# Performance work log

Measured on AMD Instinct MI355X. Metric: run time of the kernel, lower is better.

Reference implementation:

```python
import jax, jax.numpy as jnp
import numpy as np

TEMPERATURE = 1.0
N_ITER = 3
B, N_PATTERNS, N_NEURONS = 4096, 8192, 1024


def setup_inputs() -> dict:
    key = jax.random.key(0)
    kx, kp = jax.random.split(key)
    x = jax.random.normal(kx, (B, N_NEURONS), dtype=jnp.float32)
    # patterns initialized as tanh(randn * initial_variance) in the original module
    patterns = jnp.tanh(jax.random.normal(kp, (N_PATTERNS, N_NEURONS), dtype=jnp.float32) * 0.1)
    return {"x": x, "patterns": patterns}


def reference(x, patterns):
    # Iterative Hopfield update: x <- softmax(T * x @ P^T) @ P, repeated N_ITER times.
    def body(carry, _):
        scores = TEMPERATURE * jnp.einsum('bn,pn->bp', carry, patterns)  # [B, P]
        new_x = jnp.einsum('bp,pn->bn', jax.nn.softmax(scores, axis=1), patterns)  # [B, N]
        return new_x, None
    x, _ = jax.lax.scan(body, x, None, length=N_ITER)
    return x
```

## Files before the change

### kernel.cpp

```cpp
#include <hip/hip_runtime.h>
#include <hip/hip_fp16.h>
#include <stdint.h>

#define B_ROWS 4096
#define N_PAT  8192
#define N_NEU  1024

typedef _Float16 f16x8 __attribute__((ext_vector_type(8)));
typedef _Float16 f16x4 __attribute__((ext_vector_type(4)));
typedef float    f32x4 __attribute__((ext_vector_type(4)));

__device__ __forceinline__ f32x4 mfma16(f16x8 a, f16x8 b, f32x4 c) {
  return __builtin_amdgcn_mfma_f32_16x16x32_f16(a, b, c, 0, 0, 0);
}

__global__ __launch_bounds__(256) void convert_f32_f16(
    const float* __restrict__ in, _Float16* __restrict__ out, int n4) {
  int idx    = blockIdx.x * 256 + threadIdx.x;
  int stride = gridDim.x * 256;
  for (int i = idx; i < n4; i += stride) {
    float4 v = reinterpret_cast<const float4*>(in)[i];
    f16x4 h  = { (_Float16)v.x, (_Float16)v.y, (_Float16)v.z, (_Float16)v.w };
    reinterpret_cast<f16x4*>(out)[i] = h;
  }
}

__global__ __launch_bounds__(256) void transpose_f32_f16(
    const float* __restrict__ in, _Float16* __restrict__ out, int rows, int cols) {
  __shared__ float tile[32][33];
  int c0 = blockIdx.x * 32, r0 = blockIdx.y * 32;
  int tx = threadIdx.x, ty = threadIdx.y;
  #pragma unroll
  for (int i = 0; i < 32; i += 8)
    tile[ty + i][tx] = in[(size_t)(r0 + ty + i) * cols + c0 + tx];
  __syncthreads();
  #pragma unroll
  for (int i = 0; i < 32; i += 8)
    out[(size_t)(c0 + ty + i) * rows + r0 + tx] = (_Float16)tile[tx][ty + i];
}

__device__ __forceinline__ void gload_lds16(const _Float16* g, _Float16* l) {
  __builtin_amdgcn_global_load_lds(
      (const __attribute__((address_space(1))) uint32_t*)g,
      (__attribute__((address_space(3))) uint32_t*)l, 16, 0, 0);
}

template <typename OUT_T>
__global__ __launch_bounds__(512, 2) void gemm_x(
    const _Float16* __restrict__ A, const _Float16* __restrict__ Bt,
    OUT_T* __restrict__ C, int M, int N, int K, int KS) {
  __shared__ _Float16 lds[2][2][256 * 64];
  const int t    = threadIdx.x;
  const int lane = t & 63;
  const int w    = t >> 6;
  const int wr   = w >> 2;
  const int wc   = w & 3;
  const int m0   = blockIdx.x * 256;
  const int n0   = blockIdx.y * 256;
  const int k0   = blockIdx.z * KS;

  const int srow  = w * 8 + (lane >> 3);
  const int sgran = ((lane & 7) ^ ((lane >> 3) & 7)) * 8;
  const _Float16* sA = A  + (size_t)(m0 + srow) * K + sgran + k0;
  const _Float16* sB = Bt + (size_t)(n0 + srow) * K + sgran + k0;
  const size_t rj = (size_t)64 * K;
  const int ldst  = w * 512;

  const int lrow = lane & 15;
  const int kg   = lane >> 4;
  const int NT   = KS >> 6;

  f32x4 acc[8][4] = {};

  auto stage = [&](int slot, int kt) {
    #pragma unroll
    for (int j = 0; j < 4; ++j) {
      gload_lds16(sA + j * rj + kt, &lds[slot][0][j * 4096 + ldst]);
      gload_lds16(sB + j * rj + kt, &lds[slot][1][j * 4096 + ldst]);
    }
  };

  stage(0, 0);
  stage(1, 64);
  asm volatile("s_waitcnt vmcnt(8)" ::: "memory");
  __builtin_amdgcn_s_barrier();
  __builtin_amdgcn_sched_barrier(0);

  for (int tt = 0; tt < NT; ++tt) {
    const int s = tt & 1;
    const _Float16* As = lds[s][0];
    const _Float16* Bs = lds[s][1];

    f16x8 bf[4][2];
    #pragma unroll
    for (int ni = 0; ni < 4; ++ni) {
      const int br = wc * 64 + ni * 16 + lrow;
      #pragma unroll
      for (int ks = 0; ks < 2; ++ks)
        bf[ni][ks] = *reinterpret_cast<const f16x8*>(
            &Bs[br * 64 + (((ks * 4 + kg) ^ (br & 7)) * 8)]);
    }

    #pragma unroll
    for (int p = 0; p < 4; ++p) {
      f16x8 af[2][2];
      #pragma unroll
      for (int j = 0; j < 2; ++j) {
        const int ar = wr * 128 + (p * 2 + j) * 16 + lrow;
        #pragma unroll
        for (int ks = 0; ks < 2; ++ks)
          af[j][ks] = *reinterpret_cast<const f16x8*>(
              &As[ar * 64 + (((ks * 4 + kg) ^ (ar & 7)) * 8)]);
      }
      __builtin_amdgcn_s_setprio(1);
      #pragma unroll
      for (int j = 0; j < 2; ++j) {
        #pragma unroll
        for (int ni = 0; ni < 4; ++ni) {
          acc[p * 2 + j][ni] = mfma16(af[j][0], bf[ni][0], acc[p * 2 + j][ni]);
          acc[p * 2 + j][ni] = mfma16(af[j][1], bf[ni][1], acc[p * 2 + j][ni]);
        }
      }
      __builtin_amdgcn_s_setprio(0);
    }

    __builtin_amdgcn_s_barrier();
    __builtin_amdgcn_sched_barrier(0);
    if (tt + 2 < NT) {
      stage(s, (tt + 2) << 6);
      asm volatile("s_waitcnt vmcnt(8)" ::: "memory");
    } else {
      asm volatile("s_waitcnt vmcnt(0)" ::: "memory");
    }
    __builtin_amdgcn_s_barrier();
    __builtin_amdgcn_sched_barrier(0);
  }

  OUT_T* Cz = C + (size_t)blockIdx.z * M * N;
  const int crow = (lane >> 4) * 4;
  const int ccol = lane & 15;
  #pragma unroll
  for (int mi = 0; mi < 8; ++mi) {
    #pragma unroll
    for (int ni = 0; ni < 4; ++ni) {
      #pragma unroll
      for (int r = 0; r < 4; ++r) {
        int row = m0 + wr * 128 + mi * 16 + crow + r;
        int col = n0 + wc * 64 + ni * 16 + ccol;
        Cz[(size_t)row * N + col] = (OUT_T)acc[mi][ni][r];
      }
    }
  }
}

template <typename OUT_T, int SPLIT>
__global__ __launch_bounds__(256) void reduce_partials(
    const float* __restrict__ Cp, OUT_T* __restrict__ out, int n4, int stride4) {
  int idx    = blockIdx.x * 256 + threadIdx.x;
  int stride = gridDim.x * 256;
  for (int i = idx; i < n4; i += stride) {
    float4 a = reinterpret_cast<const float4*>(Cp)[i];
    #pragma unroll
    for (int s = 1; s < SPLIT; ++s) {
      float4 b = reinterpret_cast<const float4*>(Cp)[(size_t)s * stride4 + i];
      a.x += b.x; a.y += b.y; a.z += b.z; a.w += b.w;
    }
    if constexpr (sizeof(OUT_T) == 2) {
      f16x4 h = { (_Float16)a.x, (_Float16)a.y, (_Float16)a.z, (_Float16)a.w };
      reinterpret_cast<f16x4*>(out)[i] = h;
    } else {
      reinterpret_cast<float4*>(out)[i] = a;
    }
  }
}

__global__ __launch_bounds__(256) void softmax_rows(_Float16* __restrict__ S, int N) {
  const int t = threadIdx.x;
  f16x8* pv = reinterpret_cast<f16x8*>(S + (size_t)blockIdx.x * N);
  float v[32];
  float m = -3.0e38f;
  #pragma unroll
  for (int i = 0; i < 4; ++i) {
    f16x8 h = pv[i * 256 + t];
    #pragma unroll
    for (int e = 0; e < 8; ++e) {
      float f = (float)h[e];
      v[i * 8 + e] = f;
      m = fmaxf(m, f);
    }
  }
  #pragma unroll
  for (int o = 32; o; o >>= 1) m = fmaxf(m, __shfl_xor(m, o));
  __shared__ float redm[4];
  if ((t & 63) == 0) redm[t >> 6] = m;
  __syncthreads();
  m = fmaxf(fmaxf(redm[0], redm[1]), fmaxf(redm[2], redm[3]));

  float s = 0.f;
  #pragma unroll
  for (int i = 0; i < 32; ++i) { v[i] = __expf(v[i] - m); s += v[i]; }
  #pragma unroll
  for (int o = 32; o; o >>= 1) s += __shfl_xor(s, o);
  __shared__ float reds[4];
  if ((t & 63) == 0) reds[t >> 6] = s;
  __syncthreads();
  s = reds[0] + reds[1] + reds[2] + reds[3];
  const float inv = 1.0f / s;

  #pragma unroll
  for (int i = 0; i < 4; ++i) {
    f16x8 h;
    #pragma unroll
    for (int e = 0; e < 8; ++e) h[e] = (_Float16)(v[i * 8 + e] * inv);
    pv[i * 256 + t] = h;
  }
}

extern "C" void kernel_launch(void* const* d_in, const int* in_sizes, int n_in,
                              void* d_out, int out_size, void* d_ws, size_t ws_size,
                              hipStream_t stream) {
  const float* x        = (const float*)d_in[0];
  const float* patterns = (const float*)d_in[1];
  float* out            = (float*)d_out;
  char* ws = (char*)d_ws;

  _Float16* Xb   = (_Float16*)(ws);
  _Float16* Pb   = (_Float16*)(ws + ((size_t)8  << 20));
  _Float16* PbT  = (_Float16*)(ws + ((size_t)24 << 20));
  _Float16* S    = (_Float16*)(ws + ((size_t)40 << 20));
  float*    part = (float*)   (ws + ((size_t)104 << 20));

  const size_t base = (size_t)104 << 20;
  const int split = (ws_size >= base + ((size_t)64 << 20)) ? 4
                  : (ws_size >= base + ((size_t)32 << 20)) ? 2 : 1;

  convert_f32_f16<<<dim3(1024), dim3(256), 0, stream>>>(x, Xb, (B_ROWS * N_NEU) / 4);
  convert_f32_f16<<<dim3(2048), dim3(256), 0, stream>>>(patterns, Pb, (N_PAT * N_NEU) / 4);
  transpose_f32_f16<<<dim3(N_NEU / 32, N_PAT / 32), dim3(32, 8), 0, stream>>>(patterns, PbT, N_PAT, N_NEU);

  const int n4 = (B_ROWS * N_NEU) / 4;
  const int stride4 = n4;

  for (int it = 0; it < 3; ++it) {
    gemm_x<_Float16><<<dim3(B_ROWS / 256, N_PAT / 256, 1), dim3(512), 0, stream>>>(
        Xb, Pb, S, B_ROWS, N_PAT, N_NEU, N_NEU);
    softmax_rows<<<dim3(B_ROWS), dim3(256), 0, stream>>>(S, N_PAT);

    if (split > 1) {
      gemm_x<float><<<dim3(B_ROWS / 256, N_NEU / 256, split), dim3(512), 0, stream>>>(
          S, PbT, part, B_ROWS, N_NEU, N_PAT, N_PAT / split);
      if (it < 2) {
        if (split == 4)
          reduce_partials<_Float16, 4><<<dim3(2048), dim3(256), 0, stream>>>(part, Xb, n4, stride4);
        else
          reduce_partials<_Float16, 2><<<dim3(2048), dim3(256), 0, stream>>>(part, Xb, n4, stride4);
      } else {
        if (split == 4)
          reduce_partials<float, 4><<<dim3(2048), dim3(256), 0, stream>>>(part, out, n4, stride4);
        else
          reduce_partials<float, 2><<<dim3(2048), dim3(256), 0, stream>>>(part, out, n4, stride4);
      }
    } else {
      gemm_x<float><<<dim3(B_ROWS / 256, N_NEU / 256, 1), dim3(512), 0, stream>>>(
          S, PbT, part, B_ROWS, N_NEU, N_PAT, N_PAT);
      if (it < 2)
        reduce_partials<_Float16, 1><<<dim3(2048), dim3(256), 0, stream>>>(part, Xb, n4, stride4);
      else
        reduce_partials<float, 1><<<dim3(2048), dim3(256), 0, stream>>>(part, out, n4, stride4);
    }
  }
}
```

Measured before the change: 535.1 us.

## Interleave A/B tile prefetches across MFMA phases with per-phase barriers

Restructures the GEMM main loop so global-to-LDS loads for the next A tile and the tile after next for B are issued in halves between the four MFMA phases, instead of in one bulk stage after all compute. Each phase loads its A fragments, syncs with a barrier and lgkmcnt wait, then runs the MFMAs. The goal is to spread memory traffic across the compute and cut the idle time at iteration boundaries. It adds four extra barriers per K-step, and the split A/B buffering scheme overwrites buffers while other waves may still read them, which relies on the barrier placement being correct.

New measurement: 520.0 us. 2.8% less time.

```diff
diff --git a/kernel.cpp b/kernel.cpp
--- a/kernel.cpp
+++ b/kernel.cpp
@@ -72,68 +72,73 @@
 
   f32x4 acc[8][4] = {};
 
-  auto stage = [&](int slot, int kt) {
-    #pragma unroll
-    for (int j = 0; j < 4; ++j) {
-      gload_lds16(sA + j * rj + kt, &lds[slot][0][j * 4096 + ldst]);
-      gload_lds16(sB + j * rj + kt, &lds[slot][1][j * 4096 + ldst]);
-    }
+  auto stageAh = [&](int slot, int kt, int h) {
+    gload_lds16(sA + (size_t)(2 * h)     * rj + kt, &lds[slot][0][(2 * h)     * 4096 + ldst]);
+    gload_lds16(sA + (size_t)(2 * h + 1) * rj + kt, &lds[slot][0][(2 * h + 1) * 4096 + ldst]);
   };
-
-  stage(0, 0);
-  stage(1, 64);
-  asm volatile("s_waitcnt vmcnt(8)" ::: "memory");
-  __builtin_amdgcn_s_barrier();
-  __builtin_amdgcn_sched_barrier(0);
+  auto stageBh = [&](int slot, int kt, int h) {
+    gload_lds16(sB + (size_t)(2 * h)     * rj + kt, &lds[slot][1][(2 * h)     * 4096 + ldst]);
+    gload_lds16(sB + (size_t)(2 * h + 1) * rj + kt, &lds[slot][1][(2 * h + 1) * 4096 + ldst]);
+  };
+
+  stageBh(0, 0, 0);  stageBh(0, 0, 1);
+  stageAh(0, 0, 0);  stageAh(0, 0, 1);
+  stageBh(1, 64, 0); stageBh(1, 64, 1);
 
   for (int tt = 0; tt < NT; ++tt) {
     const int s = tt & 1;
+    if (tt + 1 < NT) asm volatile("s_waitcnt vmcnt(4)" ::: "memory");
+    else             asm volatile("s_waitcnt vmcnt(0)" ::: "memory");
+    __builtin_amdgcn_s_barrier();
+    __builtin_amdgcn_sched_barrier(0);
+
     const _Float16* As = lds[s][0];
     const _Float16* Bs = lds[s][1];
+    const int ktA  = (tt + 1) << 6;
+    const int ktB  = (tt + 2) << 6;
+    const bool pA  = (tt + 1 < NT);
+    const bool pB  = (tt + 2 < NT);
 
     f16x8 bf[4][2];
+
+#define PHASE_BODY(MI0)                                                              \
+    {                                                                                \
+      f16x8 a0, a1, a2, a3;                                                          \
+      { const int ar = wr * 128 + (MI0) * 16 + lrow;                                 \
+        a0 = *reinterpret_cast<const f16x8*>(&As[ar * 64 + (((kg) ^ (ar & 7)) * 8)]);      \
+        a1 = *reinterpret_cast<const f16x8*>(&As[ar * 64 + (((4 + kg) ^ (ar & 7)) * 8)]); }\
+      { const int ar = wr * 128 + ((MI0) + 1) * 16 + lrow;                           \
+        a2 = *reinterpret_cast<const f16x8*>(&As[ar * 64 + (((kg) ^ (ar & 7)) * 8)]);      \
+        a3 = *reinterpret_cast<const f16x8*>(&As[ar * 64 + (((4 + kg) ^ (ar & 7)) * 8)]); }\
+      __builtin_amdgcn_s_barrier();                                                  \
+      asm volatile("s_waitcnt lgkmcnt(0)" ::: "memory");                             \
+      __builtin_amdgcn_sched_barrier(0);                                             \
+      __builtin_amdgcn_s_setprio(1);                                                 \
+      _Pragma("unroll")                                                              \
+      for (int ni = 0; ni < 4; ++ni) {                                               \
+        acc[MI0][ni]       = mfma16(a0, bf[ni][0], acc[MI0][ni]);                    \
+        acc[MI0][ni]       = mfma16(a1, bf[ni][1], acc[MI0][ni]);                    \
+        acc[(MI0) + 1][ni] = mfma16(a2, bf[ni][0], acc[(MI0) + 1][ni]);              \
+        acc[(MI0) + 1][ni] = mfma16(a3, bf[ni][1], acc[(MI0) + 1][ni]);              \
+      }                                                                              \
+      __builtin_amdgcn_s_setprio(0);                                                 \
+    }
+
+    if (pA) stageAh(s ^ 1, ktA, 0);
     #pragma unroll
     for (int ni = 0; ni < 4; ++ni) {
       const int br = wc * 64 + ni * 16 + lrow;
-      #pragma unroll
-      for (int ks = 0; ks < 2; ++ks)
-        bf[ni][ks] = *reinterpret_cast<const f16x8*>(
-            &Bs[br * 64 + (((ks * 4 + kg) ^ (br & 7)) * 8)]);
-    }
-
-    #pragma unroll
-    for (int p = 0; p < 4; ++p) {
-      f16x8 af[2][2];
-      #pragma unroll
-      for (int j = 0; j < 2; ++j) {
-        const int ar = wr * 128 + (p * 2 + j) * 16 + lrow;
-        #pragma unroll
-        for (int ks = 0; ks < 2; ++ks)
-          af[j][ks] = *reinterpret_cast<const f16x8*>(
-              &As[ar * 64 + (((ks * 4 + kg) ^ (ar & 7)) * 8)]);
-      }
-      __builtin_amdgcn_s_setprio(1);
-      #pragma unroll
-      for (int j = 0; j < 2; ++j) {
-        #pragma unroll
-        for (int ni = 0; ni < 4; ++ni) {
-          acc[p * 2 + j][ni] = mfma16(af[j][0], bf[ni][0], acc[p * 2 + j][ni]);
-          acc[p * 2 + j][ni] = mfma16(af[j][1], bf[ni][1], acc[p * 2 + j][ni]);
-        }
-      }
-      __builtin_amdgcn_s_setprio(0);
-    }
-
-    __builtin_amdgcn_s_barrier();
-    __builtin_amdgcn_sched_barrier(0);
-    if (tt + 2 < NT) {
-      stage(s, (tt + 2) << 6);
-      asm volatile("s_waitcnt vmcnt(8)" ::: "memory");
-    } else {
-      asm volatile("s_waitcnt vmcnt(0)" ::: "memory");
-    }
-    __builtin_amdgcn_s_barrier();
-    __builtin_amdgcn_sched_barrier(0);
+      bf[ni][0] = *reinterpret_cast<const f16x8*>(&Bs[br * 64 + (((kg) ^ (br & 7)) * 8)]);
+      bf[ni][1] = *reinterpret_cast<const f16x8*>(&Bs[br * 64 + (((4 + kg) ^ (br & 7)) * 8)]);
+    }
+    PHASE_BODY(0)
+    if (pA) stageAh(s ^ 1, ktA, 1);
+    PHASE_BODY(2)
+    if (pB) stageBh(s, ktB, 0);
+    PHASE_BODY(4)
+    if (pB) stageBh(s, ktB, 1);
+    PHASE_BODY(6)
+#undef PHASE_BODY
   }
 
   OUT_T* Cz = C + (size_t)blockIdx.z * M * N;
```
